# Performance work log

Hardware: AMD Instinct MI355X
Metric: run time of the kernel (lower is better)

## Reference

```python
import jax, jax.numpy as jnp
import numpy as np

WS = (7, 7, 7)
N = WS[0] * WS[1] * WS[2]          # 343 tokens per window
B, D, L, H = 128, 512, 6, 8
DH = D // H                        # 64
DFF = 4 * D
EPS = 1e-5


def _relative_position_index_3d(ws):
    d = np.arange(ws[0]); h = np.arange(ws[1]); w = np.arange(ws[2])
    coords = np.stack(np.meshgrid(d, h, w, indexing='ij'))      # [3, D, H, W]
    cf = coords.reshape(3, -1)                                   # [3, n]
    rel = cf[:, :, None] - cf[:, None, :]                        # [3, n, n]
    rel = rel.transpose(1, 2, 0).copy()                          # [n, n, 3]
    rel[:, :, 0] += ws[0] - 1
    rel[:, :, 1] += ws[1] - 1
    rel[:, :, 2] += ws[2] - 1
    rel[:, :, 0] *= (2 * ws[1] - 1) * (2 * ws[2] - 1)
    rel[:, :, 1] *= 2 * ws[2] - 1
    return rel.sum(-1).astype(np.int32)                          # [n, n]


def setup_inputs() -> dict:
    key = jax.random.key(0)
    ks = jax.random.split(key, 16)
    s = lambda d: 1.0 / np.sqrt(d)
    inp = {
        'x':    jax.random.normal(ks[0], (B, N, D), jnp.float32),
        'Wq':   jax.random.normal(ks[1], (L, D, D), jnp.float32) * s(D),
        'Wk':   jax.random.normal(ks[2], (L, D, D), jnp.float32) * s(D),
        'Wv':   jax.random.normal(ks[3], (L, D, D), jnp.float32) * s(D),
        'Wo':   jax.random.normal(ks[4], (L, D, D), jnp.float32) * s(D),
        'W1ff': jax.random.normal(ks[5], (L, D, DFF), jnp.float32) * s(D),
        'b1ff': jnp.zeros((L, DFF), jnp.float32),
        'W2ff': jax.random.normal(ks[6], (L, DFF, D), jnp.float32) * s(DFF),
        'b2ff': jnp.zeros((L, D), jnp.float32),
        'ln1_g': jnp.ones((L, D), jnp.float32),
        'ln1_b': jnp.zeros((L, D), jnp.float32),
        'ln2_g': jnp.ones((L, D), jnp.float32),
        'ln2_b': jnp.zeros((L, D), jnp.float32),
        'lnf_g': jnp.ones((D,), jnp.float32),
        'lnf_b': jnp.zeros((D,), jnp.float32),
        'rel_table': jax.random.normal(ks[7], ((2 * WS[0] - 1) * (2 * WS[1] - 1) * (2 * WS[2] - 1), H), jnp.float32) * 0.02,
        'cpb_w1': jax.random.normal(ks[8], (H, 512), jnp.float32) * s(H),
        'cpb_b1': jax.random.normal(ks[9], (512,), jnp.float32) * 0.02,
        'cpb_w2': jax.random.normal(ks[10], (512, H), jnp.float32) * s(512),
        'rel_index': jnp.asarray(_relative_position_index_3d(WS)),
    }
    return inp


def _layer_norm(x, g, b):
    mu = jnp.mean(x, -1, keepdims=True)
    xc = x - mu
    var = jnp.mean(xc * xc, -1, keepdims=True)
    return xc * jax.lax.rsqrt(var + EPS) * g + b


def _rel_pos_bias(rel_table, cpb_w1, cpb_b1, cpb_w2, rel_index):
    # cpb_mlp: Linear(H->512) + ReLU + Linear(512->H, no bias)
    t = jax.nn.relu(rel_table @ cpb_w1 + cpb_b1) @ cpb_w2        # [T, H]
    bias = t[rel_index.reshape(-1)].reshape(N, N, H)             # gather -> [n, n, H]
    return jnp.transpose(bias, (2, 0, 1))                        # [H, n, n]


def reference(x, Wq, Wk, Wv, Wo, W1ff, b1ff, W2ff, b2ff,
              ln1_g, ln1_b, ln2_g, ln2_b, lnf_g, lnf_b,
              rel_table, cpb_w1, cpb_b1, cpb_w2, rel_index):
    bias = _rel_pos_bias(rel_table, cpb_w1, cpb_b1, cpb_w2, rel_index)  # [H, n, n] shared across layers
    scale = DH ** -0.5
    for l in range(L):
        # --- attention block (pre-norm) ---
        h = _layer_norm(x, ln1_g[l], ln1_b[l])
        q = (h @ Wq[l]).reshape(B, N, H, DH)
        k = (h @ Wk[l]).reshape(B, N, H, DH)
        v = (h @ Wv[l]).reshape(B, N, H, DH)
        scores = jnp.einsum('bihd,bjhd->bhij', q, k) * scale + bias[None]
        attn = jax.nn.softmax(scores, axis=-1)
        o = jnp.einsum('bhij,bjhd->bihd', attn, v).reshape(B, N, D)
        x = x + o @ Wo[l]
        # --- feed-forward block (pre-norm) ---
        h = _layer_norm(x, ln2_g[l], ln2_b[l])
        x = x + jax.nn.gelu(h @ W1ff[l] + b1ff[l]) @ W2ff[l] + b2ff[l]
    return _layer_norm(x, lnf_g, lnf_b)
```

## Files before the change

kernel.cpp:

```cpp
#include <hip/hip_runtime.h>

typedef __attribute__((ext_vector_type(8))) short short8;
typedef __attribute__((ext_vector_type(4))) float fx4;
typedef __attribute__((ext_vector_type(4))) int ix4;

#define MFMA16(a, b, c) __builtin_amdgcn_mfma_f32_16x16x32_bf16((a), (b), (c), 0, 0, 0)

__device__ __forceinline__ short f2bf(float f) {
  unsigned u = __float_as_uint(f);
  u += 0x7fffu + ((u >> 16) & 1u);
  return (short)(u >> 16);
}
__device__ __forceinline__ float bf2f(short v) {
  return __uint_as_float(((unsigned)(unsigned short)v) << 16);
}
__device__ __forceinline__ void glds16(const short* g, short* l) {
  __builtin_amdgcn_global_load_lds((const __attribute__((address_space(1))) void*)g,
                                   (__attribute__((address_space(3))) void*)l, 16, 0, 0);
}

__global__ __launch_bounds__(256)
void transpose_cvt(const float* __restrict__ W, short* __restrict__ Wt, int K, int N) {
  __shared__ float tile[64][65];
  const int kb = blockIdx.x * 64, nb = blockIdx.y * 64;
  const int t = threadIdx.x;
  const int tr = t >> 6, tc = t & 63;
#pragma unroll 4
  for (int i = 0; i < 16; i++) {
    int r = i * 4 + tr;
    tile[r][tc] = W[(size_t)(kb + r) * N + nb + tc];
  }
  __syncthreads();
#pragma unroll 4
  for (int i = 0; i < 16; i++) {
    int r = i * 4 + tr;
    Wt[(size_t)(nb + r) * K + kb + tc] = f2bf(tile[tc][r]);
  }
}

__global__ __launch_bounds__(256)
void cpb_kernel(const float* __restrict__ rt, const float* __restrict__ w1,
                const float* __restrict__ b1, const float* __restrict__ w2,
                float* __restrict__ tt) {
  const int id = blockIdx.x * 256 + threadIdx.x;
  if (id >= 2197 * 8) return;
  const int row = id >> 3, hh = id & 7;
  float r[8];
#pragma unroll
  for (int i = 0; i < 8; i++) r[i] = rt[row * 8 + i];
  float acc = 0.0f;
  for (int c = 0; c < 512; c++) {
    float s = b1[c];
#pragma unroll
    for (int i = 0; i < 8; i++) s += r[i] * w1[i * 512 + c];
    s = fmaxf(s, 0.0f);
    acc += s * w2[c * 8 + hh];
  }
  tt[id] = acc;
}

__global__ __launch_bounds__(256)
void build_biasfrag(const float* __restrict__ tt, const int* __restrict__ ridx,
                    short* __restrict__ biasb) {
  const int id = blockIdx.x * 256 + threadIdx.x;
  if (id >= 8 * 22 * 11 * 512) return;
  const int e = id & 7;
  const int lane = (id >> 3) & 63;
  const int rest = id >> 9;
  const int jp = rest % 11;
  const int rest2 = rest / 11;
  const int qt = rest2 % 22;
  const int h = rest2 / 22;
  const int q = qt * 16 + ((lane >> 4) << 2) + (e & 3);
  const int tok = (jp * 2 + (e >> 2)) * 16 + (lane & 15);
  float val = -1e30f;
  if (q < 343 && tok < 343) val = tt[ridx[q * 343 + tok] * 8 + h];
  biasb[id] = f2bf(val);
}

template <bool BF16OUT>
__global__ __launch_bounds__(256)
void ln_kernel(const float* x, const float* __restrict__ g,
               const float* __restrict__ bb, void* out) {
  const int row = blockIdx.x * 4 + (threadIdx.x >> 6);
  const int lane = threadIdx.x & 63;
  const float* xr = x + (size_t)row * 512 + lane * 8;
  fx4 va = *(const fx4*)xr;
  fx4 vb = *(const fx4*)(xr + 4);
  float s = va[0] + va[1] + va[2] + va[3] + vb[0] + vb[1] + vb[2] + vb[3];
#pragma unroll
  for (int d = 1; d < 64; d <<= 1) s += __shfl_xor(s, d);
  const float mu = s * (1.0f / 512.0f);
  float v[8];
#pragma unroll
  for (int i = 0; i < 4; i++) { v[i] = va[i] - mu; v[4 + i] = vb[i] - mu; }
  float s2 = 0.0f;
#pragma unroll
  for (int i = 0; i < 8; i++) s2 += v[i] * v[i];
#pragma unroll
  for (int d = 1; d < 64; d <<= 1) s2 += __shfl_xor(s2, d);
  const float rs = rsqrtf(s2 * (1.0f / 512.0f) + 1e-5f);
  fx4 ga = *(const fx4*)(g + lane * 8);
  fx4 gb = *(const fx4*)(g + lane * 8 + 4);
  fx4 ba = *(const fx4*)(bb + lane * 8);
  fx4 b2 = *(const fx4*)(bb + lane * 8 + 4);
  float o[8];
#pragma unroll
  for (int i = 0; i < 4; i++) {
    o[i] = v[i] * rs * ga[i] + ba[i];
    o[4 + i] = v[4 + i] * rs * gb[i] + b2[i];
  }
  if (BF16OUT) {
    short8 ov;
#pragma unroll
    for (int i = 0; i < 8; i++) ov[i] = f2bf(o[i]);
    *(short8*)((short*)out + (size_t)row * 512 + lane * 8) = ov;
  } else {
    float* op = (float*)out + (size_t)row * 512 + lane * 8;
    fx4 o1, o2;
#pragma unroll
    for (int i = 0; i < 4; i++) { o1[i] = o[i]; o2[i] = o[4 + i]; }
    *(fx4*)op = o1;
    *(fx4*)(op + 4) = o2;
  }
}

template <int EPI>
__global__ __launch_bounds__(256)
void gemm128(const short* __restrict__ A, const short* __restrict__ Bt,
             int N, int K, int nbn, int scaleN,
             const float* __restrict__ bias, const float* xres, void* out) {
  __shared__ short Al[8192];
  __shared__ short Bl[8192];
  const int nwg = gridDim.x;
  const int orig = blockIdx.x;
  const int qq = nwg >> 3, rr = nwg & 7, xc = orig & 7, o8 = orig >> 3;
  const int wgid = (xc < rr ? xc * (qq + 1) : rr * (qq + 1) + (xc - rr) * qq) + o8;
  const int m0 = (wgid / nbn) * 128, n0 = (wgid % nbn) * 128;
  const int t = threadIdx.x;
  const int lane = t & 63, wv = t >> 6;
  const int wm = (wv >> 1) * 64, wn = (wv & 1) * 64;
  const int lr = lane & 15, lg = lane >> 4;
  const int srow = wv * 32 + (lane >> 2);
  const int skk = (lane & 3) * 8;
  const short* ag0 = A + (size_t)(m0 + srow) * K + skk;
  const short* ag1 = A + (size_t)(m0 + srow + 16) * K + skk;
  const short* bg0 = Bt + (size_t)(n0 + srow) * K + skk;
  const short* bg1 = Bt + (size_t)(n0 + srow + 16) * K + skk;
  const int nkt = K >> 5;
  fx4 acc[4][4] = {};
#define STAGE(KT, BUF)                                   \
  do {                                                   \
    const int off_ = (KT) * 32;                          \
    short* la_ = Al + (BUF) * 4096 + wv * 1024;          \
    short* lb_ = Bl + (BUF) * 4096 + wv * 1024;          \
    glds16(ag0 + off_, la_);                             \
    glds16(ag1 + off_, la_ + 512);                       \
    glds16(bg0 + off_, lb_);                             \
    glds16(bg1 + off_, lb_ + 512);                       \
  } while (0)
  STAGE(0, 0);
  __syncthreads();
  int buf = 0;
  for (int kt = 0; kt < nkt; kt++) {
    if (kt + 1 < nkt) STAGE(kt + 1, buf ^ 1);
    short8 af[4], bf[4];
#pragma unroll
    for (int i = 0; i < 4; i++)
      af[i] = *(const short8*)&Al[buf * 4096 + (wm + i * 16 + lr) * 32 + lg * 8];
#pragma unroll
    for (int i = 0; i < 4; i++)
      bf[i] = *(const short8*)&Bl[buf * 4096 + (wn + i * 16 + lr) * 32 + lg * 8];
#pragma unroll
    for (int mi = 0; mi < 4; mi++)
#pragma unroll
      for (int ni = 0; ni < 4; ni++)
        acc[mi][ni] = MFMA16(af[mi], bf[ni], acc[mi][ni]);
    __syncthreads();
    buf ^= 1;
  }
#undef STAGE
#pragma unroll
  for (int mi = 0; mi < 4; mi++) {
#pragma unroll
    for (int ni = 0; ni < 4; ni++) {
#pragma unroll
      for (int r = 0; r < 4; r++) {
        const int row = m0 + wm + mi * 16 + lg * 4 + r;
        const int col = n0 + wn + ni * 16 + lr;
        const float vacc = acc[mi][ni][r];
        const size_t idx = (size_t)row * N + col;
        if (EPI == 0) {
          const float sc = (col < scaleN) ? 0.125f : 1.0f;
          ((short*)out)[idx] = f2bf(vacc * sc);
        } else if (EPI == 1) {
          ((float*)out)[idx] = xres[idx] + vacc;
        } else if (EPI == 2) {
          const float v = vacc + bias[col];
          const float tt = v * v;
          const float u2 = v * fmaf(tt, -0.0713548165f, -1.5957691216f);
          const float g = v * __builtin_amdgcn_rcpf(1.0f + __expf(u2));
          ((short*)out)[idx] = f2bf(g);
        } else {
          ((float*)out)[idx] = xres[idx] + vacc + bias[col];
        }
      }
    }
  }
}

__global__ __launch_bounds__(512, 1)
void attn_kernel(const short* __restrict__ qkv, const short* __restrict__ biasb,
                 short* __restrict__ obuf) {
  __shared__ short Kl[352][72];
  __shared__ short Vt[64][360];
  __shared__ short Pl[8][16][96];
  const int b = blockIdx.x >> 3, h = blockIdx.x & 7;
  const int t = threadIdx.x, lane = t & 63, wv = t >> 6;
  const int lr = lane & 15, lg = lane >> 4;
  const size_t base = (size_t)b * 343 * 1536 + h * 64;
  const short* qg = qkv + base;
  const short* kg = qkv + base + 512;
  const short* vg = qkv + base + 1024;
  for (int c = t; c < 352 * 8; c += 512) {
    const int tok = c >> 3, d8 = (c & 7) * 8;
    const int ts = tok < 343 ? tok : 342;
    short8 kvv = *(const short8*)(kg + (size_t)ts * 1536 + d8);
    short8 vvv = *(const short8*)(vg + (size_t)ts * 1536 + d8);
    *(short8*)&Kl[tok][d8] = kvv;
#pragma unroll
    for (int j = 0; j < 8; j++) Vt[d8 + j][tok] = vvv[j];
  }
  __syncthreads();
  for (int qt = wv; qt < 22; qt += 8) {
    const int q0 = qt * 16;
    const int qr = q0 + lr;
    const int qs = qr < 343 ? qr : 342;
    short8 qf0 = *(const short8*)(qg + (size_t)qs * 1536 + lg * 8);
    short8 qf1 = *(const short8*)(qg + (size_t)qs * 1536 + 32 + lg * 8);
    fx4 s[22];
#pragma unroll
    for (int j = 0; j < 22; j++) {
      short8 kf0 = *(const short8*)&Kl[j * 16 + lr][lg * 8];
      short8 kf1 = *(const short8*)&Kl[j * 16 + lr][32 + lg * 8];
      fx4 z = {0.0f, 0.0f, 0.0f, 0.0f};
      z = MFMA16(qf0, kf0, z);
      z = MFMA16(qf1, kf1, z);
      s[j] = z;
    }
    const short* bp = biasb + (size_t)((h * 22 + qt) * 11) * 512 + lane * 8;
#pragma unroll
    for (int jp = 0; jp < 11; jp++) {
      short8 bb = *(const short8*)(bp + jp * 512);
#pragma unroll
      for (int r = 0; r < 4; r++) {
        s[2 * jp][r] += bf2f(bb[r]);
        s[2 * jp + 1][r] += bf2f(bb[4 + r]);
      }
    }
    float mx[4] = {-1e30f, -1e30f, -1e30f, -1e30f};
#pragma unroll
    for (int j = 0; j < 22; j++)
#pragma unroll
      for (int r = 0; r < 4; r++) mx[r] = fmaxf(mx[r], s[j][r]);
#pragma unroll
    for (int r = 0; r < 4; r++) {
      float m = mx[r];
      m = fmaxf(m, __shfl_xor(m, 1));
      m = fmaxf(m, __shfl_xor(m, 2));
      m = fmaxf(m, __shfl_xor(m, 4));
      m = fmaxf(m, __shfl_xor(m, 8));
      mx[r] = m;
    }
    float sm[4] = {0.0f, 0.0f, 0.0f, 0.0f};
#pragma unroll
    for (int j = 0; j < 22; j++)
#pragma unroll
      for (int r = 0; r < 4; r++) {
        const float p = __expf(s[j][r] - mx[r]);
        s[j][r] = p;
        sm[r] += p;
      }
#pragma unroll
    for (int r = 0; r < 4; r++) {
      float ss = sm[r];
      ss += __shfl_xor(ss, 1);
      ss += __shfl_xor(ss, 2);
      ss += __shfl_xor(ss, 4);
      ss += __shfl_xor(ss, 8);
      sm[r] = 1.0f / ss;
    }
    fx4 oacc[4] = {};
#pragma unroll
    for (int c = 0; c < 4; c++) {
      const int nj = (c < 3) ? 6 : 4;
#pragma unroll
      for (int j = 0; j < 6; j++) {
        if (j < nj) {
#pragma unroll
          for (int r = 0; r < 4; r++)
            Pl[wv][lg * 4 + r][j * 16 + lr] = f2bf(s[c * 6 + j][r] * sm[r]);
        }
      }
      const int nk = (c < 3) ? 3 : 2;
#pragma unroll
      for (int ks = 0; ks < 3; ks++) {
        if (ks < nk) {
          short8 pb = *(const short8*)&Pl[wv][lr][ks * 32 + lg * 8];
#pragma unroll
          for (int mi = 0; mi < 4; mi++) {
            short8 vva = *(const short8*)&Vt[mi * 16 + lr][c * 96 + ks * 32 + lg * 8];
            oacc[mi] = MFMA16(vva, pb, oacc[mi]);
          }
        }
      }
    }
    if (qr < 343) {
#pragma unroll
      for (int mi = 0; mi < 4; mi++)
#pragma unroll
        for (int r = 0; r < 4; r++) {
          const int dh = mi * 16 + lg * 4 + r;
          obuf[(size_t)(b * 343 + qr) * 512 + h * 64 + dh] = f2bf(oacc[mi][r]);
        }
    }
  }
}

extern "C" void kernel_launch(void* const* d_in, const int* in_sizes, int n_in,
                              void* d_out, int out_size, void* d_ws, size_t ws_size,
                              hipStream_t stream) {
  const float* x_in = (const float*)d_in[0];
  const float* Wq = (const float*)d_in[1];
  const float* Wk = (const float*)d_in[2];
  const float* Wv = (const float*)d_in[3];
  const float* Wo = (const float*)d_in[4];
  const float* W1 = (const float*)d_in[5];
  const float* b1 = (const float*)d_in[6];
  const float* W2 = (const float*)d_in[7];
  const float* b2 = (const float*)d_in[8];
  const float* ln1g = (const float*)d_in[9];
  const float* ln1b = (const float*)d_in[10];
  const float* ln2g = (const float*)d_in[11];
  const float* ln2b = (const float*)d_in[12];
  const float* lnfg = (const float*)d_in[13];
  const float* lnfb = (const float*)d_in[14];
  const float* rtab = (const float*)d_in[15];
  const float* cw1 = (const float*)d_in[16];
  const float* cb1 = (const float*)d_in[17];
  const float* cw2 = (const float*)d_in[18];
  const int* ridx = (const int*)d_in[19];
  float* xout = (float*)d_out;

  char* p = (char*)d_ws;
  short* wt = (short*)p;      p += 37748736;
  short* hbuf = (short*)p;    p += 44957696;
  char* big = p;              p += 179830784;
  short* biasb = (short*)p;   p += 1982464;
  float* tt = (float*)p;      p += 70304;
  short* qkvbuf = (short*)big;
  short* obuf = (short*)(big + 134873088);
  short* mid = (short*)big;

  cpb_kernel<<<(2197 * 8 + 255) / 256, 256, 0, stream>>>(rtab, cw1, cb1, cw2, tt);
  build_biasfrag<<<(8 * 22 * 11 * 512 + 255) / 256, 256, 0, stream>>>(tt, ridx, biasb);

  for (int l = 0; l < 6; l++) {
    const size_t wl = (size_t)l * 3145728;
    transpose_cvt<<<dim3(8, 8), 256, 0, stream>>>(Wq + (size_t)l * 262144, wt + wl, 512, 512);
    transpose_cvt<<<dim3(8, 8), 256, 0, stream>>>(Wk + (size_t)l * 262144, wt + wl + 262144, 512, 512);
    transpose_cvt<<<dim3(8, 8), 256, 0, stream>>>(Wv + (size_t)l * 262144, wt + wl + 524288, 512, 512);
    transpose_cvt<<<dim3(8, 8), 256, 0, stream>>>(Wo + (size_t)l * 262144, wt + wl + 786432, 512, 512);
    transpose_cvt<<<dim3(8, 32), 256, 0, stream>>>(W1 + (size_t)l * 1048576, wt + wl + 1048576, 512, 2048);
    transpose_cvt<<<dim3(32, 8), 256, 0, stream>>>(W2 + (size_t)l * 1048576, wt + wl + 2097152, 2048, 512);
  }

  for (int l = 0; l < 6; l++) {
    const size_t wl = (size_t)l * 3145728;
    const float* xsrc = (l == 0) ? x_in : xout;
    ln_kernel<true><<<10976, 256, 0, stream>>>(xsrc, ln1g + l * 512, ln1b + l * 512, hbuf);
    gemm128<0><<<343 * 12, 256, 0, stream>>>(hbuf, wt + wl, 1536, 512, 12, 512, nullptr, nullptr, qkvbuf);
    attn_kernel<<<1024, 512, 0, stream>>>(qkvbuf, biasb, obuf);
    gemm128<1><<<343 * 4, 256, 0, stream>>>(obuf, wt + wl + 786432, 512, 512, 4, 0, nullptr, xsrc, xout);
    ln_kernel<true><<<10976, 256, 0, stream>>>(xout, ln2g + l * 512, ln2b + l * 512, hbuf);
    gemm128<2><<<343 * 16, 256, 0, stream>>>(hbuf, wt + wl + 1048576, 2048, 512, 16, 0, b1 + l * 2048, nullptr, mid);
    gemm128<3><<<343 * 4, 256, 0, stream>>>(mid, wt + wl + 2097152, 512, 2048, 4, 0, b2 + l * 512, xout, xout);
  }
  ln_kernel<false><<<10976, 256, 0, stream>>>(xout, lnfg, lnfb, xout);
}
```

Baseline: 4.254 ms.

## Templatize GEMM with 256x256 tiles, K=64 stages and swizzled LDS

Replaces the fixed 128x128 GEMM with a templated kernel. It uses 256x256 tiles with 8 waves for the QKV and FFN1 projections, keeps 128x128 for the output and FFN2 projections, and doubles the K step per stage to 64. An XOR swizzle is added to the LDS layout to avoid bank conflicts, and a row clamp plus guarded stores handle the ragged last M tile. The larger tiles raise operand reuse and cut LDS and global traffic per MFMA. The cost is more LDS per block (64KB) and more registers, which lowers occupancy, plus some wasted work in the partial last tile.

```diff
diff --git a/kernel.cpp b/kernel.cpp
--- a/kernel.cpp
+++ b/kernel.cpp
@@ -125,69 +125,93 @@
   }
 }
 
-template <int EPI>
-__global__ __launch_bounds__(256)
-void gemm128(const short* __restrict__ A, const short* __restrict__ Bt,
-             int N, int K, int nbn, int scaleN,
-             const float* __restrict__ bias, const float* xres, void* out) {
-  __shared__ short Al[8192];
-  __shared__ short Bl[8192];
+template <int BM, int BN, int NWM, int NWN, int EPI>
+__global__ __launch_bounds__(NWM* NWN * 64)
+void gemm_t(const short* __restrict__ A, const short* __restrict__ Bt,
+            int M, int N, int K, int nbn, int scaleN,
+            const float* __restrict__ bias, const float* xres, void* out) {
+  constexpr int NW = NWM * NWN;
+  constexpr int MF = BM / NWM / 16;
+  constexpr int NF = BN / NWN / 16;
+  __shared__ short Al[2 * BM * 64];
+  __shared__ short Bl[2 * BN * 64];
   const int nwg = gridDim.x;
   const int orig = blockIdx.x;
   const int qq = nwg >> 3, rr = nwg & 7, xc = orig & 7, o8 = orig >> 3;
   const int wgid = (xc < rr ? xc * (qq + 1) : rr * (qq + 1) + (xc - rr) * qq) + o8;
-  const int m0 = (wgid / nbn) * 128, n0 = (wgid % nbn) * 128;
-  const int t = threadIdx.x;
-  const int lane = t & 63, wv = t >> 6;
-  const int wm = (wv >> 1) * 64, wn = (wv & 1) * 64;
+  const int m0 = (wgid / nbn) * BM, n0 = (wgid % nbn) * BN;
+  const int t = threadIdx.x, lane = t & 63, wv = t >> 6;
+  const int wave_m = wv / NWN, wave_n = wv % NWN;
   const int lr = lane & 15, lg = lane >> 4;
-  const int srow = wv * 32 + (lane >> 2);
-  const int skk = (lane & 3) * 8;
-  const short* ag0 = A + (size_t)(m0 + srow) * K + skk;
-  const short* ag1 = A + (size_t)(m0 + srow + 16) * K + skk;
-  const short* bg0 = Bt + (size_t)(n0 + srow) * K + skk;
-  const short* bg1 = Bt + (size_t)(n0 + srow + 16) * K + skk;
-  const int nkt = K >> 5;
-  fx4 acc[4][4] = {};
-#define STAGE(KT, BUF)                                   \
-  do {                                                   \
-    const int off_ = (KT) * 32;                          \
-    short* la_ = Al + (BUF) * 4096 + wv * 1024;          \
-    short* lb_ = Bl + (BUF) * 4096 + wv * 1024;          \
-    glds16(ag0 + off_, la_);                             \
-    glds16(ag1 + off_, la_ + 512);                       \
-    glds16(bg0 + off_, lb_);                             \
-    glds16(bg1 + off_, lb_ + 512);                       \
+  const int scol = ((lane & 3) * 8) ^ ((lane & 32) ? 16 : 0);
+  const short* apt[4];
+  const short* bpt[4];
+#pragma unroll
+  for (int r = 0; r < 4; r++) {
+    const int c = r * NW + wv;
+    const int rg = c >> 1, cg = c & 1;
+    int rowA = m0 + rg * 16 + (lane >> 2);
+    if (rowA > M - 1) rowA = M - 1;
+    apt[r] = A + (size_t)rowA * K + cg * 32 + scol;
+    const int rowB = n0 + rg * 16 + (lane >> 2);
+    bpt[r] = Bt + (size_t)rowB * K + cg * 32 + scol;
+  }
+  const int cswz = (lg * 8) ^ ((lr & 8) ? 16 : 0);
+  int aoff[MF], boff[NF];
+#pragma unroll
+  for (int mi = 0; mi < MF; mi++) aoff[mi] = (wave_m * MF + mi) * 1024 + lr * 32 + cswz;
+#pragma unroll
+  for (int ni = 0; ni < NF; ni++) boff[ni] = (wave_n * NF + ni) * 1024 + lr * 32 + cswz;
+  fx4 acc[MF][NF];
+#pragma unroll
+  for (int mi = 0; mi < MF; mi++)
+#pragma unroll
+    for (int ni = 0; ni < NF; ni++) acc[mi][ni] = fx4{0.f, 0.f, 0.f, 0.f};
+#define STAGE(BUF)                                              \
+  do {                                                          \
+    short* la_ = Al + (BUF) * (BM * 64) + wv * 512;             \
+    short* lb_ = Bl + (BUF) * (BN * 64) + wv * 512;             \
+    _Pragma("unroll") for (int r_ = 0; r_ < 4; r_++) {          \
+      glds16(apt[r_], la_ + r_ * NW * 512);                     \
+      glds16(bpt[r_], lb_ + r_ * NW * 512);                     \
+      apt[r_] += 64;                                            \
+      bpt[r_] += 64;                                            \
+    }                                                           \
   } while (0)
-  STAGE(0, 0);
+  const int nkt = K >> 6;
+  STAGE(0);
   __syncthreads();
   int buf = 0;
   for (int kt = 0; kt < nkt; kt++) {
-    if (kt + 1 < nkt) STAGE(kt + 1, buf ^ 1);
-    short8 af[4], bf[4];
-#pragma unroll
-    for (int i = 0; i < 4; i++)
-      af[i] = *(const short8*)&Al[buf * 4096 + (wm + i * 16 + lr) * 32 + lg * 8];
-#pragma unroll
-    for (int i = 0; i < 4; i++)
-      bf[i] = *(const short8*)&Bl[buf * 4096 + (wn + i * 16 + lr) * 32 + lg * 8];
-#pragma unroll
-    for (int mi = 0; mi < 4; mi++)
-#pragma unroll
-      for (int ni = 0; ni < 4; ni++)
-        acc[mi][ni] = MFMA16(af[mi], bf[ni], acc[mi][ni]);
+    if (kt + 1 < nkt) STAGE(buf ^ 1);
+    const int boA = buf * (BM * 64);
+    const int boB = buf * (BN * 64);
+#pragma unroll
+    for (int ks = 0; ks < 2; ks++) {
+      short8 af[MF], bf[NF];
+#pragma unroll
+      for (int mi = 0; mi < MF; mi++) af[mi] = *(const short8*)&Al[boA + aoff[mi] + ks * 512];
+#pragma unroll
+      for (int ni = 0; ni < NF; ni++) bf[ni] = *(const short8*)&Bl[boB + boff[ni] + ks * 512];
+#pragma unroll
+      for (int mi = 0; mi < MF; mi++)
+#pragma unroll
+        for (int ni = 0; ni < NF; ni++)
+          acc[mi][ni] = MFMA16(af[mi], bf[ni], acc[mi][ni]);
+    }
     __syncthreads();
     buf ^= 1;
   }
 #undef STAGE
 #pragma unroll
-  for (int mi = 0; mi < 4; mi++) {
-#pragma unroll
-    for (int ni = 0; ni < 4; ni++) {
+  for (int mi = 0; mi < MF; mi++) {
+#pragma unroll
+    for (int ni = 0; ni < NF; ni++) {
 #pragma unroll
       for (int r = 0; r < 4; r++) {
-        const int row = m0 + wm + mi * 16 + lg * 4 + r;
-        const int col = n0 + wn + ni * 16 + lr;
+        const int row = m0 + wave_m * MF * 16 + mi * 16 + lg * 4 + r;
+        const int col = n0 + wave_n * NF * 16 + ni * 16 + lr;
+        if (BM > 128 && row >= M) continue;
         const float vacc = acc[mi][ni][r];
         const size_t idx = (size_t)row * N + col;
         if (EPI == 0) {
@@ -362,6 +386,8 @@
   short* obuf = (short*)(big + 134873088);
   short* mid = (short*)big;
 
+  const int M = 43904;
+
   cpb_kernel<<<(2197 * 8 + 255) / 256, 256, 0, stream>>>(rtab, cw1, cb1, cw2, tt);
   build_biasfrag<<<(8 * 22 * 11 * 512 + 255) / 256, 256, 0, stream>>>(tt, ridx, biasb);
 
@@ -379,12 +405,16 @@
     const size_t wl = (size_t)l * 3145728;
     const float* xsrc = (l == 0) ? x_in : xout;
     ln_kernel<true><<<10976, 256, 0, stream>>>(xsrc, ln1g + l * 512, ln1b + l * 512, hbuf);
-    gemm128<0><<<343 * 12, 256, 0, stream>>>(hbuf, wt + wl, 1536, 512, 12, 512, nullptr, nullptr, qkvbuf);
+    gemm_t<256, 256, 2, 4, 0><<<172 * 6, 512, 0, stream>>>(
+        hbuf, wt + wl, M, 1536, 512, 6, 512, nullptr, nullptr, qkvbuf);
     attn_kernel<<<1024, 512, 0, stream>>>(qkvbuf, biasb, obuf);
-    gemm128<1><<<343 * 4, 256, 0, stream>>>(obuf, wt + wl + 786432, 512, 512, 4, 0, nullptr, xsrc, xout);
+    gemm_t<128, 128, 2, 2, 1><<<343 * 4, 256, 0, stream>>>(
+        obuf, wt + wl + 786432, M, 512, 512, 4, 0, nullptr, xsrc, xout);
     ln_kernel<true><<<10976, 256, 0, stream>>>(xout, ln2g + l * 512, ln2b + l * 512, hbuf);
-    gemm128<2><<<343 * 16, 256, 0, stream>>>(hbuf, wt + wl + 1048576, 2048, 512, 16, 0, b1 + l * 2048, nullptr, mid);
-    gemm128<3><<<343 * 4, 256, 0, stream>>>(mid, wt + wl + 2097152, 512, 2048, 4, 0, b2 + l * 512, xout, xout);
+    gemm_t<256, 256, 2, 4, 2><<<172 * 8, 512, 0, stream>>>(
+        hbuf, wt + wl + 1048576, M, 2048, 512, 8, 0, b1 + l * 2048, nullptr, mid);
+    gemm_t<128, 128, 2, 2, 3><<<343 * 4, 256, 0, stream>>>(
+        mid, wt + wl + 2097152, M, 512, 2048, 4, 0, b2 + l * 512, xout, xout);
   }
   ln_kernel<false><<<10976, 256, 0, stream>>>(xout, lnfg, lnfb, xout);
 }
```

Result: slower. 5.261 ms (+23.7%).
